# Optimization experiments

Hardware: AMD Instinct MI355X
Metric: run time of the kernel (lower is better)

## Reference

```python
import jax, jax.numpy as jnp
import numpy as np

B, S, N, D, H, M, P_OFF = 16, 4, 2048, 128, 16, 4096, 4092


def setup_inputs() -> dict:
    key = jax.random.key(0)
    ks = jax.random.split(key, 6)
    return {
        "X": jax.random.normal(ks[0], (B, S, N), dtype=jnp.float32),
        "W_q": jax.random.normal(ks[1], (N, N), dtype=jnp.float32) * 0.02,
        "W_k": jax.random.normal(ks[2], (N, N), dtype=jnp.float32) * 0.02,
        "W_v": jax.random.normal(ks[3], (N, N), dtype=jnp.float32) * 0.02,
        "cache_K": jax.random.normal(ks[4], (B, H, M, D), dtype=jnp.float32),
        "cache_V": jax.random.normal(ks[5], (B, H, M, D), dtype=jnp.float32),
        "P": P_OFF,
    }


def reference(X, W_q, W_k, W_v, cache_K, cache_V, P):
    b, s, n = X.shape
    _, h, m, d = cache_K.shape
    # RMSNorm (no eps, no learned scale, matching the source)
    variance = jnp.mean(X * X, axis=-1, keepdims=True)
    X_norm = X * jax.lax.rsqrt(variance)
    # QKV projections -> [b, h, s, d]
    Q = (X_norm @ W_q).reshape(b, s, h, d).transpose(0, 2, 1, 3)
    K = (X_norm @ W_k).reshape(b, s, h, d).transpose(0, 2, 1, 3)
    V = (X_norm @ W_v).reshape(b, s, h, d).transpose(0, 2, 1, 3)
    # KV-cache write at static offset P
    cK = cache_K.at[:, :, P:P + s, :].set(K)
    cV = cache_V.at[:, :, P:P + s, :].set(V)
    # Attention over full cache (note: source applies no 1/sqrt(d) scale)
    scores = jnp.einsum("bhsd,bhmd->bhsm", Q, cK)
    attn = jax.nn.softmax(scores, axis=-1)
    O = jnp.einsum("bhsm,bhmd->bhsd", attn, cV)
    return O.transpose(0, 2, 1, 3).reshape(b, s, n)
```

## Files before the change

kernel.cpp:

```cpp
#include <hip/hip_runtime.h>
#include <hip/hip_bf16.h>
#include <math.h>

#define NB 16
#define NS 4
#define NN 2048
#define ND 128
#define NH 16
#define NM 4096
#define NCHK 4
#define CHROWS 1024
#define TROWS 32
#define NT 32
#define NKC 16

#define SC_OFF   0u
#define Q_OFF    131072u
#define K_OFF    262144u
#define V_OFF    393216u
#define OP_OFF   524288u
#define ML_OFF   1572864u
#define PART_OFF 1589248u

__global__ __launch_bounds__(256) void k_rmsnorm(const float* __restrict__ X,
                                                 float* __restrict__ ws) {
    const int row = blockIdx.x;
    const int tid = threadIdx.x;
    const float* xr = X + (size_t)row * NN;
    float4 a = *(const float4*)(xr + tid * 4);
    float4 b = *(const float4*)(xr + 1024 + tid * 4);
    float ss = a.x*a.x + a.y*a.y + a.z*a.z + a.w*a.w
             + b.x*b.x + b.y*b.y + b.z*b.z + b.w*b.w;
    #pragma unroll
    for (int off = 32; off; off >>= 1) ss += __shfl_xor(ss, off);
    __shared__ float ls[4];
    if ((tid & 63) == 0) ls[tid >> 6] = ss;
    __syncthreads();
    if (tid == 0)
        ws[SC_OFF + row] = rsqrtf((ls[0] + ls[1] + ls[2] + ls[3]) * (1.0f / NN));
}

__global__ __launch_bounds__(256) void k_qkv(const float* __restrict__ X,
                                             const float* __restrict__ Wq,
                                             const float* __restrict__ Wk,
                                             const float* __restrict__ Wv,
                                             float* __restrict__ ws) {
    __shared__ float xsT[64][68];
    __shared__ float wt[64][132];
    const int ct    = blockIdx.x;
    const int which = blockIdx.y;
    const int kc    = blockIdx.z;
    const float* __restrict__ W = (which == 0) ? Wq : (which == 1) ? Wk : Wv;
    const int tid = threadIdx.x;
    const int c0  = ct * 128;
    const int rg  = tid >> 5;
    const int cg  = tid & 31;
    const float scl = ws[SC_OFF + (tid >> 2)];

    float4 acc[8];
    #pragma unroll
    for (int i = 0; i < 8; i++) acc[i] = make_float4(0.f, 0.f, 0.f, 0.f);

    for (int s = 0; s < 2; s++) {
        const int k0 = kc * 128 + s * 64;
        __syncthreads();
        {
            const int r  = tid >> 2;
            const int q4 = tid & 3;
            #pragma unroll
            for (int i = 0; i < 4; i++) {
                const int f4 = q4 + i * 4;
                float4 v = *(const float4*)(X + (size_t)r * NN + k0 + f4 * 4);
                xsT[f4 * 4 + 0][r] = v.x * scl;
                xsT[f4 * 4 + 1][r] = v.y * scl;
                xsT[f4 * 4 + 2][r] = v.z * scl;
                xsT[f4 * 4 + 3][r] = v.w * scl;
            }
        }
        {
            #pragma unroll
            for (int j8 = 0; j8 < 8; j8++) {
                const int kk  = j8 * 8 + (tid >> 5);
                const int f4c = tid & 31;
                float4 v = *(const float4*)(W + (size_t)(k0 + kk) * NN + c0 + f4c * 4);
                *(float4*)&wt[kk][f4c * 4] = v;
            }
        }
        __syncthreads();
        #pragma unroll 8
        for (int kk = 0; kk < 64; kk++) {
            const float4 x0 = *(const float4*)&xsT[kk][rg * 8];
            const float4 x1 = *(const float4*)&xsT[kk][rg * 8 + 4];
            const float4 w4 = *(const float4*)&wt[kk][cg * 4];
            acc[0].x += x0.x*w4.x; acc[0].y += x0.x*w4.y; acc[0].z += x0.x*w4.z; acc[0].w += x0.x*w4.w;
            acc[1].x += x0.y*w4.x; acc[1].y += x0.y*w4.y; acc[1].z += x0.y*w4.z; acc[1].w += x0.y*w4.w;
            acc[2].x += x0.z*w4.x; acc[2].y += x0.z*w4.y; acc[2].z += x0.z*w4.z; acc[2].w += x0.z*w4.w;
            acc[3].x += x0.w*w4.x; acc[3].y += x0.w*w4.y; acc[3].z += x0.w*w4.z; acc[3].w += x0.w*w4.w;
            acc[4].x += x1.x*w4.x; acc[4].y += x1.x*w4.y; acc[4].z += x1.x*w4.z; acc[4].w += x1.x*w4.w;
            acc[5].x += x1.y*w4.x; acc[5].y += x1.y*w4.y; acc[5].z += x1.y*w4.z; acc[5].w += x1.y*w4.w;
            acc[6].x += x1.z*w4.x; acc[6].y += x1.z*w4.y; acc[6].z += x1.z*w4.z; acc[6].w += x1.z*w4.w;
            acc[7].x += x1.w*w4.x; acc[7].y += x1.w*w4.y; acc[7].z += x1.w*w4.z; acc[7].w += x1.w*w4.w;
        }
    }
    float* po = ws + PART_OFF + (size_t)(kc * 3 + which) * 131072u;
    #pragma unroll
    for (int i = 0; i < 8; i++)
        *(float4*)(po + (size_t)(rg * 8 + i) * NN + c0 + cg * 4) = acc[i];
}

__global__ __launch_bounds__(256) void k_reduce(float* __restrict__ ws) {
    const int idx = blockIdx.x * 256 + threadIdx.x;
    const int which = idx >> 15;
    const int off   = idx & 32767;
    float4 s = make_float4(0.f, 0.f, 0.f, 0.f);
    #pragma unroll
    for (int kcc = 0; kcc < NKC; kcc++) {
        const float4 v = *(const float4*)(ws + PART_OFF
                         + (size_t)(kcc * 3 + which) * 131072u + (size_t)off * 4);
        s.x += v.x; s.y += v.y; s.z += v.z; s.w += v.w;
    }
    *(float4*)(ws + Q_OFF + (size_t)which * 131072u + (size_t)off * 4) = s;
}

__global__ __launch_bounds__(256) void k_attn(const float* __restrict__ cK,
                                              const float* __restrict__ cV,
                                              const int* __restrict__ Pp,
                                              float* __restrict__ ws) {
    const int ch = blockIdx.x, h = blockIdx.y, b = blockIdx.z;
    const int tid = threadIdx.x;
    const int wv = tid >> 6, lane = tid & 63;
    const int half = lane >> 5, r32 = lane & 31;
    const int P = *Pp;
    __shared__ float Ks[2][TROWS * 128];
    __shared__ float Vs[2][TROWS * 128];
    __shared__ float ps[TROWS][4] __attribute__((aligned(16)));
    __shared__ float facs[4] __attribute__((aligned(16)));
    __shared__ float Ow[4][4][128];
    __shared__ float mls[4][2];

    const float* qrow = ws + Q_OFF + (size_t)(b * 4 + wv) * NN + h * 128 + half * 64;
    float4 qreg[16];
    #pragma unroll
    for (int j = 0; j < 16; j++) qreg[j] = *(const float4*)(qrow + j * 4);

    const float* kbase = cK + (size_t)(b * NH + h) * NM * ND;
    const float* vbase = cV + (size_t)(b * NH + h) * NM * ND;
    const float* knew  = ws + K_OFF;
    const float* vnew  = ws + V_OFF;
    const int mb0 = ch * CHROWS;

    auto STAGE = [&](int tt, int bufi) {
        const int mb = mb0 + tt * TROWS;
        if (wv < 2) {
            #pragma unroll
            for (int i = 0; i < 8; i++) {
                const int g0  = (wv * 8 + i) * 64;
                const int g   = g0 + lane;
                const int row = g >> 5;
                const int c4  = g & 31;
                const int csw = c4 ^ (row & 7);
                const int mrow = mb + row;
                const float* src = (mrow >= P && mrow < P + NS)
                    ? knew + (size_t)(b * 4 + (mrow - P)) * NN + h * 128 + csw * 4
                    : kbase + (size_t)mrow * ND + csw * 4;
                __builtin_amdgcn_global_load_lds(
                    (const __attribute__((address_space(1))) void*)src,
                    (__attribute__((address_space(3))) void*)(&Ks[bufi][g0 * 4]),
                    16, 0, 0);
            }
        } else {
            #pragma unroll
            for (int i = 0; i < 8; i++) {
                const int g0  = ((wv - 2) * 8 + i) * 64;
                const int g   = g0 + lane;
                const int row = g >> 5;
                const int c4  = g & 31;
                const int mrow = mb + row;
                const float* src = (mrow >= P && mrow < P + NS)
                    ? vnew + (size_t)(b * 4 + (mrow - P)) * NN + h * 128 + c4 * 4
                    : vbase + (size_t)mrow * ND + c4 * 4;
                __builtin_amdgcn_global_load_lds(
                    (const __attribute__((address_space(1))) void*)src,
                    (__attribute__((address_space(3))) void*)(&Vs[bufi][g0 * 4]),
                    16, 0, 0);
            }
        }
    };

    float m_run = -INFINITY, l_run = 0.f;
    float2 Oa[4];
    #pragma unroll
    for (int q = 0; q < 4; q++) Oa[q] = make_float2(0.f, 0.f);

    STAGE(0, 0);

    for (int t = 0; t < NT; t++) {
        const int cur = t & 1;
        asm volatile("s_waitcnt vmcnt(0) lgkmcnt(0)" ::: "memory");
        __builtin_amdgcn_s_barrier();
        __builtin_amdgcn_sched_barrier(0);

        if (t + 1 < NT) STAGE(t + 1, cur ^ 1);

        const int s7 = r32 & 7;
        const float* kr = &Ks[cur][r32 * 128 + half * 64];
        float s = 0.f;
        #pragma unroll
        for (int j = 0; j < 16; j++) {
            const float4 k4 = *(const float4*)&kr[(j ^ s7) * 4];
            const float4 q4 = qreg[j];
            s += k4.x*q4.x + k4.y*q4.y + k4.z*q4.z + k4.w*q4.w;
        }
        s += __shfl_xor(s, 32);
        float wm = s;
        #pragma unroll
        for (int off = 16; off; off >>= 1) wm = fmaxf(wm, __shfl_xor(wm, off));
        const float mn  = fmaxf(m_run, wm);
        const float fac = __expf(m_run - mn);
        m_run = mn;
        const float p = __expf(s - mn);
        l_run = l_run * fac + ((half == 0) ? p : 0.f);
        if (half == 0) ps[r32][wv] = p;
        if (lane == 0) facs[wv] = fac;

        asm volatile("s_waitcnt lgkmcnt(0)" ::: "memory");
        __builtin_amdgcn_s_barrier();
        __builtin_amdgcn_sched_barrier(0);

        const float4 fq = *(const float4*)&facs[0];
        Oa[0].x *= fq.x; Oa[0].y *= fq.x;
        Oa[1].x *= fq.y; Oa[1].y *= fq.y;
        Oa[2].x *= fq.z; Oa[2].y *= fq.z;
        Oa[3].x *= fq.w; Oa[3].y *= fq.w;
        const int r0 = wv * 8;
        #pragma unroll
        for (int rr = 0; rr < 8; rr++) {
            const float2 v2 = *(const float2*)&Vs[cur][(r0 + rr) * 128 + lane * 2];
            const float4 pr = *(const float4*)&ps[r0 + rr][0];
            Oa[0].x += pr.x * v2.x; Oa[0].y += pr.x * v2.y;
            Oa[1].x += pr.y * v2.x; Oa[1].y += pr.y * v2.y;
            Oa[2].x += pr.z * v2.x; Oa[2].y += pr.z * v2.y;
            Oa[3].x += pr.w * v2.x; Oa[3].y += pr.w * v2.y;
        }
    }

    #pragma unroll
    for (int off = 32; off; off >>= 1) l_run += __shfl_xor(l_run, off);
    #pragma unroll
    for (int q = 0; q < 4; q++)
        *(float2*)&Ow[wv][q][lane * 2] = Oa[q];
    if (lane == 0) { mls[wv][0] = m_run; mls[wv][1] = l_run; }
    __syncthreads();

    const int q = wv;
    const int d0 = lane * 2;
    float o0 = 0.f, o1 = 0.f;
    #pragma unroll
    for (int w2 = 0; w2 < 4; w2++) {
        o0 += Ow[w2][q][d0];
        o1 += Ow[w2][q][d0 + 1];
    }
    const size_t bh = (size_t)(b * NH + h);
    const size_t pidx = ((bh * NCHK + ch) * 4 + q) * 128 + d0;
    ws[OP_OFF + pidx]     = o0;
    ws[OP_OFF + pidx + 1] = o1;
    if (lane == 0) {
        const size_t mi = ((bh * NCHK + ch) * 4 + q) * 2;
        ws[ML_OFF + mi]     = mls[q][0];
        ws[ML_OFF + mi + 1] = mls[q][1];
    }
}

__global__ __launch_bounds__(256) void k_comb(const float* __restrict__ ws,
                                              float* __restrict__ out) {
    const int bh = blockIdx.x;
    const int b = bh >> 4, h = bh & 15;
    const int tid = threadIdx.x;
    const int q = tid >> 6, d0 = (tid & 63) * 2;
    float ms = -INFINITY;
    #pragma unroll
    for (int c = 0; c < NCHK; c++)
        ms = fmaxf(ms, ws[ML_OFF + (((size_t)bh * NCHK + c) * 4 + q) * 2]);
    float o0 = 0.f, o1 = 0.f, den = 0.f;
    #pragma unroll
    for (int c = 0; c < NCHK; c++) {
        const size_t mi = (((size_t)bh * NCHK + c) * 4 + q) * 2;
        float e = __expf(ws[ML_OFF + mi] - ms);
        den += e * ws[ML_OFF + mi + 1];
        const size_t pi = (((size_t)bh * NCHK + c) * 4 + q) * 128 + d0;
        o0 += e * ws[OP_OFF + pi];
        o1 += e * ws[OP_OFF + pi + 1];
    }
    const float inv = 1.0f / den;
    const size_t oi = (size_t)(b * 4 + q) * NN + h * 128 + d0;
    *(float2*)(out + oi) = make_float2(o0 * inv, o1 * inv);
}

extern "C" void kernel_launch(void* const* d_in, const int* in_sizes, int n_in,
                              void* d_out, int out_size, void* d_ws, size_t ws_size,
                              hipStream_t stream) {
    const float* X  = (const float*)d_in[0];
    const float* Wq = (const float*)d_in[1];
    const float* Wk = (const float*)d_in[2];
    const float* Wv = (const float*)d_in[3];
    const float* cK = (const float*)d_in[4];
    const float* cV = (const float*)d_in[5];
    const int*   Pp = (const int*)d_in[6];
    float* ws = (float*)d_ws;
    float* out = (float*)d_out;

    hipLaunchKernelGGL(k_rmsnorm, dim3(64), dim3(256), 0, stream, X, ws);
    hipLaunchKernelGGL(k_qkv, dim3(16, 3, NKC), dim3(256), 0, stream, X, Wq, Wk, Wv, ws);
    hipLaunchKernelGGL(k_reduce, dim3(384), dim3(256), 0, stream, ws);
    hipLaunchKernelGGL(k_attn, dim3(NCHK, NH, NB), dim3(256), 0, stream, cK, cV, Pp, ws);
    hipLaunchKernelGGL(k_comb, dim3(NB * NH), dim3(256), 0, stream, ws, out);
}
```

Baseline: 233.7 us.

## Give each wave its own query's PV product and drop the intra-tile barrier

The attention kernel now has each wave accumulate the full output row for its own query. It broadcasts the softmax weights across lanes with shuffles instead of exchanging them through shared memory, which removes the second barrier per tile and the cross-wave reduction at the end. Each wave now reads the whole V tile from LDS, about four times the LDS traffic for V. The split over the cache is also halved to 2 chunks of 2048 rows, which halves the block count and the partial results the combine kernel has to merge. Since the kernel streams about 1 GB of cache, it is likely near bandwidth-bound, so the gain is uncertain.

```diff
diff --git a/kernel.cpp b/kernel.cpp
--- a/kernel.cpp
+++ b/kernel.cpp
@@ -8,10 +8,10 @@
 #define ND 128
 #define NH 16
 #define NM 4096
-#define NCHK 4
-#define CHROWS 1024
+#define NCHK 2
+#define CHROWS 2048
 #define TROWS 32
-#define NT 32
+#define NT 64
 #define NKC 16
 
 #define SC_OFF   0u
@@ -133,10 +133,6 @@
     const int P = *Pp;
     __shared__ float Ks[2][TROWS * 128];
     __shared__ float Vs[2][TROWS * 128];
-    __shared__ float ps[TROWS][4] __attribute__((aligned(16)));
-    __shared__ float facs[4] __attribute__((aligned(16)));
-    __shared__ float Ow[4][4][128];
-    __shared__ float mls[4][2];
 
     const float* qrow = ws + Q_OFF + (size_t)(b * 4 + wv) * NN + h * 128 + half * 64;
     float4 qreg[16];
@@ -188,9 +184,7 @@
     };
 
     float m_run = -INFINITY, l_run = 0.f;
-    float2 Oa[4];
-    #pragma unroll
-    for (int q = 0; q < 4; q++) Oa[q] = make_float2(0.f, 0.f);
+    float O0 = 0.f, O1 = 0.f;
 
     STAGE(0, 0);
 
@@ -219,55 +213,28 @@
         const float fac = __expf(m_run - mn);
         m_run = mn;
         const float p = __expf(s - mn);
-        l_run = l_run * fac + ((half == 0) ? p : 0.f);
-        if (half == 0) ps[r32][wv] = p;
-        if (lane == 0) facs[wv] = fac;
-
-        asm volatile("s_waitcnt lgkmcnt(0)" ::: "memory");
-        __builtin_amdgcn_s_barrier();
-        __builtin_amdgcn_sched_barrier(0);
-
-        const float4 fq = *(const float4*)&facs[0];
-        Oa[0].x *= fq.x; Oa[0].y *= fq.x;
-        Oa[1].x *= fq.y; Oa[1].y *= fq.y;
-        Oa[2].x *= fq.z; Oa[2].y *= fq.z;
-        Oa[3].x *= fq.w; Oa[3].y *= fq.w;
-        const int r0 = wv * 8;
-        #pragma unroll
-        for (int rr = 0; rr < 8; rr++) {
-            const float2 v2 = *(const float2*)&Vs[cur][(r0 + rr) * 128 + lane * 2];
-            const float4 pr = *(const float4*)&ps[r0 + rr][0];
-            Oa[0].x += pr.x * v2.x; Oa[0].y += pr.x * v2.y;
-            Oa[1].x += pr.y * v2.x; Oa[1].y += pr.y * v2.y;
-            Oa[2].x += pr.z * v2.x; Oa[2].y += pr.z * v2.y;
-            Oa[3].x += pr.w * v2.x; Oa[3].y += pr.w * v2.y;
+        l_run = l_run * fac + p;
+
+        O0 *= fac; O1 *= fac;
+        const float* vp = &Vs[cur][lane * 2];
+        #pragma unroll 8
+        for (int r = 0; r < 32; r++) {
+            const float pr = __shfl(p, r);
+            const float2 v2 = *(const float2*)(vp + r * 128);
+            O0 += pr * v2.x;
+            O1 += pr * v2.y;
         }
     }
 
     #pragma unroll
     for (int off = 32; off; off >>= 1) l_run += __shfl_xor(l_run, off);
-    #pragma unroll
-    for (int q = 0; q < 4; q++)
-        *(float2*)&Ow[wv][q][lane * 2] = Oa[q];
-    if (lane == 0) { mls[wv][0] = m_run; mls[wv][1] = l_run; }
-    __syncthreads();
-
-    const int q = wv;
-    const int d0 = lane * 2;
-    float o0 = 0.f, o1 = 0.f;
-    #pragma unroll
-    for (int w2 = 0; w2 < 4; w2++) {
-        o0 += Ow[w2][q][d0];
-        o1 += Ow[w2][q][d0 + 1];
-    }
-    const size_t bh = (size_t)(b * NH + h);
-    const size_t pidx = ((bh * NCHK + ch) * 4 + q) * 128 + d0;
-    ws[OP_OFF + pidx]     = o0;
-    ws[OP_OFF + pidx + 1] = o1;
+    l_run *= 0.5f;
+
+    const size_t base = (((size_t)(b * NH + h) * NCHK + ch) * 4 + wv);
+    *(float2*)(ws + OP_OFF + base * 128 + lane * 2) = make_float2(O0, O1);
     if (lane == 0) {
-        const size_t mi = ((bh * NCHK + ch) * 4 + q) * 2;
-        ws[ML_OFF + mi]     = mls[q][0];
-        ws[ML_OFF + mi + 1] = mls[q][1];
+        ws[ML_OFF + base * 2]     = m_run;
+        ws[ML_OFF + base * 2 + 1] = l_run;
     }
 }
 
```

New measurement: 249.7 us. 1.07x slower.
